# Kernel optimization log

Hardware: AMD Instinct MI355X
Metric: run time of the kernel (lower is better)

## Reference

```python
import jax, jax.numpy as jnp
import numpy as np

N_HEADS = 12

def setup_inputs() -> dict:
    key = jax.random.key(0)
    k1, k2, k3 = jax.random.split(key, 3)
    B, N, D = 2, 2048, 768
    x = jax.random.normal(k1, (B, N, D), dtype=jnp.float32)
    # Linear weights stored as [in, out] (equivalent to torch W.T)
    Wkqv = jax.random.normal(k2, (D, 3 * D), dtype=jnp.float32) * (1.0 / np.sqrt(D))
    bkqv = jnp.zeros((3 * D,), dtype=jnp.float32)
    Wproj = jax.random.normal(k3, (D, D), dtype=jnp.float32) * (1.0 / np.sqrt(D))
    bproj = jnp.zeros((D,), dtype=jnp.float32)
    return {"x": x, "Wkqv": Wkqv, "bkqv": bkqv, "Wproj": Wproj, "bproj": bproj}


def reference(x, Wkqv, bkqv, Wproj, bproj):
    B, N, D = x.shape
    H = N_HEADS
    hd = D // H
    kqv = x @ Wkqv + bkqv                     # [B, N, 3D]
    # NOTE: original chunks in (k, q, v) order
    k, q, v = jnp.split(kqv, 3, axis=-1)
    k = k.reshape(B, N, H, hd).transpose(0, 2, 1, 3)   # [B, H, N, hd]
    q = q.reshape(B, N, H, hd).transpose(0, 2, 1, 3)
    v = v.reshape(B, N, H, hd).transpose(0, 2, 1, 3)
    att = jnp.einsum('bhqd,bhkd->bhqk', q, k) / jnp.sqrt(jnp.float32(hd))
    causal = jnp.tril(jnp.ones((N, N), dtype=bool))    # [N, N]
    att = jnp.where(causal[None, None, :, :], att, jnp.float32(-jnp.inf))
    w = jax.nn.softmax(att, axis=-1)
    sa = jnp.einsum('bhqk,bhkd->bhqd', w, v)           # [B, H, N, hd]
    sa = sa.transpose(0, 2, 1, 3).reshape(B, N, D)
    return sa @ Wproj + bproj
```

## Files before the change

### kernel.cpp

```cpp
#include <hip/hip_runtime.h>

typedef __attribute__((ext_vector_type(8))) short bf16x8;
typedef __attribute__((ext_vector_type(4))) float f32x4;
typedef __attribute__((ext_vector_type(16))) float f32x16;

#define BATCH 2
#define SEQ 2048
#define DMODEL 768
#define NH 12
#define HD 64
#define M_TOK (BATCH * SEQ)
#define N_KQV (3 * DMODEL)

#define GLOAD16(gsrc, ldst) __builtin_amdgcn_global_load_lds( \
    (const __attribute__((address_space(1))) unsigned int*)(const void*)(gsrc), \
    (__attribute__((address_space(3))) unsigned int*)(void*)(ldst), 16, 0, 0)

__device__ __forceinline__ unsigned short f2bf(float f) {
  unsigned int u = __float_as_uint(f);
  u += 0x7FFFu + ((u >> 16) & 1u);
  return (unsigned short)(u >> 16);
}

__device__ __forceinline__ unsigned int cvtpk(float lo, float hi) {
  unsigned int r;
  asm("v_cvt_pk_bf16_f32 %0, %1, %2" : "=v"(r) : "v"(lo), "v"(hi));
  return r;
}


__global__ void cvt_f32_bf16(const float* __restrict__ in,
                             unsigned short* __restrict__ out, int n4) {
  int i = blockIdx.x * blockDim.x + threadIdx.x;
  if (i >= n4) return;
  float4 v = reinterpret_cast<const float4*>(in)[i];
  unsigned long long p = (unsigned long long)f2bf(v.x)
                       | ((unsigned long long)f2bf(v.y) << 16)
                       | ((unsigned long long)f2bf(v.z) << 32)
                       | ((unsigned long long)f2bf(v.w) << 48);
  reinterpret_cast<unsigned long long*>(out)[i] = p;
}

__global__ void transpose_cvt(const float* __restrict__ in,
                              unsigned short* __restrict__ out,
                              int rows, int cols) {
  __shared__ float tile[32][33];
  int c0 = blockIdx.x * 32, r0 = blockIdx.y * 32;
  for (int i = threadIdx.y; i < 32; i += 8)
    tile[i][threadIdx.x] = in[(size_t)(r0 + i) * cols + c0 + threadIdx.x];
  __syncthreads();
  for (int i = threadIdx.y; i < 32; i += 8)
    out[(size_t)(c0 + i) * rows + r0 + threadIdx.x] = f2bf(tile[threadIdx.x][i]);
}

template <int MODE>
__global__ __launch_bounds__(256) void gemm_bt(
    const unsigned short* __restrict__ A,
    const unsigned short* __restrict__ BT,
    const float* __restrict__ bias,
    int M, int N, int K,
    unsigned short* __restrict__ outK, unsigned short* __restrict__ outQ,
    unsigned short* __restrict__ outVT, float* __restrict__ outF) {
  __shared__ __align__(16) unsigned short lds_a[2][128][32];
  __shared__ __align__(16) unsigned short lds_b[2][128][32];
  const int tid = threadIdx.x;
  const int lane = tid & 63;
  const int w = tid >> 6;
  const int wm = w >> 1, wn = w & 1;
  const int l15 = lane & 15, lg = lane >> 4;
  const int m0 = blockIdx.y * 128, n0 = blockIdx.x * 128;

  f32x4 acc[4][4];
#pragma unroll
  for (int i = 0; i < 4; i++)
#pragma unroll
    for (int jj = 0; jj < 4; jj++) acc[i][jj] = (f32x4){0.f, 0.f, 0.f, 0.f};

  const int grow = lane >> 2;
  const int gcol = (lane & 3) * 8;

  const int KT = K >> 5;

#define STAGE_TILE(buf, k0)                                                  \
  {                                                                          \
    const size_t a0 = (size_t)(m0 + w * 32 + grow) * K + (k0) + gcol;        \
    const size_t b0 = (size_t)(n0 + w * 32 + grow) * K + (k0) + gcol;        \
    GLOAD16(&A[a0],                  &lds_a[buf][w * 32][0]);                \
    GLOAD16(&A[a0 + 16 * (size_t)K], &lds_a[buf][w * 32 + 16][0]);           \
    GLOAD16(&BT[b0],                 &lds_b[buf][w * 32][0]);                \
    GLOAD16(&BT[b0 + 16 * (size_t)K], &lds_b[buf][w * 32 + 16][0]);          \
  }

  STAGE_TILE(0, 0);
  __syncthreads();

  for (int kt = 0; kt < KT; ++kt) {
    const int cur = kt & 1;
    if (kt + 1 < KT) STAGE_TILE(cur ^ 1, (kt + 1) << 5);
    bf16x8 af[4], bfr[4];
#pragma unroll
    for (int mi = 0; mi < 4; mi++)
      af[mi] = *(const bf16x8*)&lds_a[cur][wm * 64 + mi * 16 + l15][lg * 8];
#pragma unroll
    for (int ni = 0; ni < 4; ni++)
      bfr[ni] = *(const bf16x8*)&lds_b[cur][wn * 64 + ni * 16 + l15][lg * 8];
#pragma unroll
    for (int mi = 0; mi < 4; mi++)
#pragma unroll
      for (int ni = 0; ni < 4; ni++)
        acc[mi][ni] = __builtin_amdgcn_mfma_f32_16x16x32_bf16(af[mi], bfr[ni], acc[mi][ni], 0, 0, 0);
    __syncthreads();
  }
#undef STAGE_TILE

#pragma unroll
  for (int mi = 0; mi < 4; mi++) {
#pragma unroll
    for (int ni = 0; ni < 4; ni++) {
#pragma unroll
      for (int r = 0; r < 4; r++) {
        int row = m0 + wm * 64 + mi * 16 + lg * 4 + r;
        int col = n0 + wn * 64 + ni * 16 + l15;
        float v = acc[mi][ni][r] + bias[col];
        if (MODE == 0) {
          int chunk = col / DMODEL;
          int d = col - chunk * DMODEL;
          int hh = d >> 6, di = d & 63;
          int bb = row >> 11, tok = row & 2047;
          int bh = bb * NH + hh;
          if (chunk == 0)
            outK[((size_t)bh * SEQ + tok) * HD + di] = f2bf(v);
          else if (chunk == 1)
            outQ[((size_t)bh * SEQ + tok) * HD + di] = f2bf(v * 0.125f);
          else
            outVT[((size_t)bh * HD + di) * SEQ + tok] = f2bf(v);
        } else {
          outF[(size_t)row * N + col] = v;
        }
      }
    }
  }
}

__global__ __launch_bounds__(128) void attn_kernel(
    const unsigned short* __restrict__ qbuf,
    const unsigned short* __restrict__ kbuf,
    const unsigned short* __restrict__ vT,
    unsigned short* __restrict__ sa) {
  __shared__ __align__(16) char smem_raw[18432];
  auto k_lds = reinterpret_cast<unsigned short (*)[72]>(smem_raw);
  auto v_lds = reinterpret_cast<unsigned short (*)[72]>(smem_raw + 9216);
  auto o_merge = reinterpret_cast<float (*)[32][33]>(smem_raw);
  auto l_merge = reinterpret_cast<float (*)[32]>(smem_raw + 9216);

  const int tid = threadIdx.x, lane = tid & 63, w = tid >> 6;
  const int l31 = lane & 31, hi = lane >> 5;

  const int fid = (int)blockIdx.y * (int)gridDim.x + (int)blockIdx.x;
  const int xcd = fid & 7, slot = fid >> 3;
  const int bh = ((slot >> 6) << 3) + xcd;
  const int t = 63 - (slot & 63);
  const int ktmax = t >> 1;

  const size_t qk_base = (size_t)bh * SEQ * HD;
  const size_t v_base = (size_t)bh * HD * SEQ;
  const int bb = bh / NH, h = bh - bb * NH;

  const int sr = w * 32 + (lane >> 3);
  const int sc = (lane & 7) * 8;

  {
    bf16x8 rk[4], rv[4];
#pragma unroll
    for (int p = 0; p < 4; p++) {
      rk[p] = *(const bf16x8*)&kbuf[qk_base + (size_t)(sr + 8 * p) * HD + sc];
      rv[p] = *(const bf16x8*)&vT[v_base + (size_t)(sr + 8 * p) * SEQ + sc];
    }
#pragma unroll
    for (int p = 0; p < 4; p++) {
      *(bf16x8*)&k_lds[sr + 8 * p][sc] = rk[p];
      *(bf16x8*)&v_lds[sr + 8 * p][sc] = rv[p];
    }
  }

  bf16x8 aq[4];
#pragma unroll
  for (int ds = 0; ds < 4; ds++)
    aq[ds] = *(const bf16x8*)&qbuf[qk_base + (size_t)(t * 32 + l31) * HD + ds * 16 + hi * 8];

  f32x16 o0, o1;
#pragma unroll
  for (int i = 0; i < 16; i++) { o0[i] = 0.f; o1[i] = 0.f; }
  float lsum = 0.f;

  __syncthreads();

  for (int kt = 0; kt <= ktmax; ++kt) {
    const bool more = (kt < ktmax);
    bf16x8 rk[4], rv[4];
    if (more) {
      const int nrow = (kt + 1) * 64;
#pragma unroll
      for (int p = 0; p < 4; p++) {
        rk[p] = *(const bf16x8*)&kbuf[qk_base + (size_t)(nrow + sr + 8 * p) * HD + sc];
        rv[p] = *(const bf16x8*)&vT[v_base + (size_t)(sr + 8 * p) * SEQ + nrow + sc];
      }
    }

    f32x16 s;
#pragma unroll
    for (int i = 0; i < 16; i++) s[i] = 0.f;
    __builtin_amdgcn_s_setprio(1);
#pragma unroll
    for (int ds = 0; ds < 4; ds++) {
      bf16x8 bk = *(const bf16x8*)&k_lds[w * 32 + l31][ds * 16 + hi * 8];
      s = __builtin_amdgcn_mfma_f32_32x32x16_bf16(bk, aq[ds], s, 0, 0, 0);
    }
    __builtin_amdgcn_s_setprio(0);

    const bool diag = (kt == ktmax);
    const int qb2 = (t & 1) * 32;
#pragma unroll
    for (int r = 0; r < 16; r++) {
      int kr = (r & 3) + 8 * (r >> 2) + 4 * hi;
      float val = s[r];
      if (diag && (w * 32 + kr > qb2 + l31)) val = -1e30f;
      float p = __expf(val);
      s[r] = p;
      lsum += p;
    }

    union { unsigned int u[4]; bf16x8 v; } f1, f2;
    {
      unsigned int A = cvtpk(s[0], s[1]), B = cvtpk(s[2], s[3]);
      unsigned int C = cvtpk(s[4], s[5]), D = cvtpk(s[6], s[7]);
      auto rAC = __builtin_amdgcn_permlane32_swap(A, C, false, false);
      auto rBD = __builtin_amdgcn_permlane32_swap(B, D, false, false);
      f1.u[0] = rAC[0]; f1.u[1] = rBD[0]; f1.u[2] = rAC[1]; f1.u[3] = rBD[1];
      unsigned int A2 = cvtpk(s[8], s[9]),   B2 = cvtpk(s[10], s[11]);
      unsigned int C2 = cvtpk(s[12], s[13]), D2 = cvtpk(s[14], s[15]);
      auto rAC2 = __builtin_amdgcn_permlane32_swap(A2, C2, false, false);
      auto rBD2 = __builtin_amdgcn_permlane32_swap(B2, D2, false, false);
      f2.u[0] = rAC2[0]; f2.u[1] = rBD2[0]; f2.u[2] = rAC2[1]; f2.u[3] = rBD2[1];
    }

    __builtin_amdgcn_s_setprio(1);
    {
      bf16x8 bv00 = *(const bf16x8*)&v_lds[l31][w * 32 + hi * 8];
      bf16x8 bv01 = *(const bf16x8*)&v_lds[32 + l31][w * 32 + hi * 8];
      o0 = __builtin_amdgcn_mfma_f32_32x32x16_bf16(f1.v, bv00, o0, 0, 0, 0);
      o1 = __builtin_amdgcn_mfma_f32_32x32x16_bf16(f1.v, bv01, o1, 0, 0, 0);
      bf16x8 bv10 = *(const bf16x8*)&v_lds[l31][w * 32 + 16 + hi * 8];
      bf16x8 bv11 = *(const bf16x8*)&v_lds[32 + l31][w * 32 + 16 + hi * 8];
      o0 = __builtin_amdgcn_mfma_f32_32x32x16_bf16(f2.v, bv10, o0, 0, 0, 0);
      o1 = __builtin_amdgcn_mfma_f32_32x32x16_bf16(f2.v, bv11, o1, 0, 0, 0);
    }
    __builtin_amdgcn_s_setprio(0);

    if (more) {
      __syncthreads();
#pragma unroll
      for (int p = 0; p < 4; p++) {
        *(bf16x8*)&k_lds[sr + 8 * p][sc] = rk[p];
        *(bf16x8*)&v_lds[sr + 8 * p][sc] = rv[p];
      }
      __syncthreads();
    }
  }

  __syncthreads();
  {
    float ltot = lsum + __shfl_xor(lsum, 32);
    if (hi == 0) l_merge[w][l31] = ltot;
    f32x16 osend = w ? o0 : o1;
#pragma unroll
    for (int r = 0; r < 16; r++) {
      int ql = (r & 3) + 8 * (r >> 2) + 4 * hi;
      o_merge[w][ql][l31] = osend[r];
    }
    __syncthreads();
    f32x16 okeep = w ? o1 : o0;
#pragma unroll
    for (int r = 0; r < 16; r++) {
      int ql = (r & 3) + 8 * (r >> 2) + 4 * hi;
      float ot = okeep[r] + o_merge[1 - w][ql][l31];
      float lt = l_merge[0][ql] + l_merge[1][ql];
      sa[((size_t)bb * SEQ + t * 32 + ql) * DMODEL + h * HD + w * 32 + l31] = f2bf(ot / lt);
    }
  }
}


extern "C" void kernel_launch(void* const* d_in, const int* in_sizes, int n_in,
                              void* d_out, int out_size, void* d_ws, size_t ws_size,
                              hipStream_t stream) {
  const float* x     = (const float*)d_in[0];
  const float* Wkqv  = (const float*)d_in[1];
  const float* bkqv  = (const float*)d_in[2];
  const float* Wproj = (const float*)d_in[3];
  const float* bproj = (const float*)d_in[4];
  float* out = (float*)d_out;

  char* ws = (char*)d_ws;
  unsigned short* x_bf   = (unsigned short*)(ws + 0);
  unsigned short* wkqvT  = (unsigned short*)(ws + 6291456);
  unsigned short* wprojT = (unsigned short*)(ws + 9830400);
  unsigned short* qb     = (unsigned short*)(ws + 11010048);
  unsigned short* kb     = (unsigned short*)(ws + 17301504);
  unsigned short* vT     = (unsigned short*)(ws + 23592960);
  unsigned short* sa     = (unsigned short*)(ws + 29884416);

  cvt_f32_bf16<<<(M_TOK * DMODEL / 4 + 255) / 256, 256, 0, stream>>>(x, x_bf, M_TOK * DMODEL / 4);
  transpose_cvt<<<dim3(N_KQV / 32, DMODEL / 32), dim3(32, 8), 0, stream>>>(Wkqv, wkqvT, DMODEL, N_KQV);
  transpose_cvt<<<dim3(DMODEL / 32, DMODEL / 32), dim3(32, 8), 0, stream>>>(Wproj, wprojT, DMODEL, DMODEL);

  gemm_bt<0><<<dim3(N_KQV / 128, M_TOK / 128), 256, 0, stream>>>(
      x_bf, wkqvT, bkqv, M_TOK, N_KQV, DMODEL, kb, qb, vT, nullptr);

  attn_kernel<<<dim3(64, BATCH * NH), 128, 0, stream>>>(qb, kb, vT, sa);

  gemm_bt<1><<<dim3(DMODEL / 128, M_TOK / 128), 256, 0, stream>>>(
      sa, wprojT, bproj, M_TOK, DMODEL, DMODEL, nullptr, nullptr, nullptr, out);
}
```

Measured before the change: 113.2 us.

## Give each wave its own 32 query rows and double-buffer K/V tiles in LDS

Restructures the attention kernel so each block handles 64 query rows, with each of two waves owning 32 rows and iterating over both 32-key halves of every 64-key tile. This replaces the old key-split across waves and removes the end-of-kernel cross-wave merge of O and row sums. K/V tiles are now double-buffered in LDS, cutting one barrier per iteration, and fully masked diagonal sub-tiles are skipped. The grid halves to 768 blocks, which lowers parallelism and uses more LDS per block.

```diff
diff --git a/kernel.cpp b/kernel.cpp
--- a/kernel.cpp
+++ b/kernel.cpp
@@ -147,20 +147,19 @@
     const unsigned short* __restrict__ kbuf,
     const unsigned short* __restrict__ vT,
     unsigned short* __restrict__ sa) {
-  __shared__ __align__(16) char smem_raw[18432];
-  auto k_lds = reinterpret_cast<unsigned short (*)[72]>(smem_raw);
-  auto v_lds = reinterpret_cast<unsigned short (*)[72]>(smem_raw + 9216);
-  auto o_merge = reinterpret_cast<float (*)[32][33]>(smem_raw);
-  auto l_merge = reinterpret_cast<float (*)[32]>(smem_raw + 9216);
+  __shared__ __align__(16) unsigned short k_lds[2][64][72];
+  __shared__ __align__(16) unsigned short v_lds[2][64][72];
+  __shared__ float l_sh[2][32];
 
   const int tid = threadIdx.x, lane = tid & 63, w = tid >> 6;
   const int l31 = lane & 31, hi = lane >> 5;
 
   const int fid = (int)blockIdx.y * (int)gridDim.x + (int)blockIdx.x;
   const int xcd = fid & 7, slot = fid >> 3;
-  const int bh = ((slot >> 6) << 3) + xcd;
-  const int t = 63 - (slot & 63);
-  const int ktmax = t >> 1;
+  const int head3 = slot % 3;
+  const int t = 31 - slot / 3;
+  const int bh = head3 * 8 + xcd;
+  const int ktmax = t;
 
   const size_t qk_base = (size_t)bh * SEQ * HD;
   const size_t v_base = (size_t)bh * HD * SEQ;
@@ -178,25 +177,28 @@
     }
 #pragma unroll
     for (int p = 0; p < 4; p++) {
-      *(bf16x8*)&k_lds[sr + 8 * p][sc] = rk[p];
-      *(bf16x8*)&v_lds[sr + 8 * p][sc] = rv[p];
+      *(bf16x8*)&k_lds[0][sr + 8 * p][sc] = rk[p];
+      *(bf16x8*)&v_lds[0][sr + 8 * p][sc] = rv[p];
     }
   }
 
   bf16x8 aq[4];
 #pragma unroll
   for (int ds = 0; ds < 4; ds++)
-    aq[ds] = *(const bf16x8*)&qbuf[qk_base + (size_t)(t * 32 + l31) * HD + ds * 16 + hi * 8];
+    aq[ds] = *(const bf16x8*)&qbuf[qk_base + (size_t)(t * 64 + w * 32 + l31) * HD + ds * 16 + hi * 8];
 
   f32x16 o0, o1;
 #pragma unroll
   for (int i = 0; i < 16; i++) { o0[i] = 0.f; o1[i] = 0.f; }
-  float lsum = 0.f;
+  float ls0 = 0.f, ls1 = 0.f;
 
   __syncthreads();
 
   for (int kt = 0; kt <= ktmax; ++kt) {
+    const int cur = kt & 1;
     const bool more = (kt < ktmax);
+    const bool diag = (kt == ktmax);
+
     bf16x8 rk[4], rv[4];
     if (more) {
       const int nrow = (kt + 1) * 64;
@@ -207,85 +209,81 @@
       }
     }
 
-    f32x16 s;
-#pragma unroll
-    for (int i = 0; i < 16; i++) s[i] = 0.f;
-    __builtin_amdgcn_s_setprio(1);
-#pragma unroll
-    for (int ds = 0; ds < 4; ds++) {
-      bf16x8 bk = *(const bf16x8*)&k_lds[w * 32 + l31][ds * 16 + hi * 8];
-      s = __builtin_amdgcn_mfma_f32_32x32x16_bf16(bk, aq[ds], s, 0, 0, 0);
-    }
-    __builtin_amdgcn_s_setprio(0);
-
-    const bool diag = (kt == ktmax);
-    const int qb2 = (t & 1) * 32;
-#pragma unroll
-    for (int r = 0; r < 16; r++) {
-      int kr = (r & 3) + 8 * (r >> 2) + 4 * hi;
-      float val = s[r];
-      if (diag && (w * 32 + kr > qb2 + l31)) val = -1e30f;
-      float p = __expf(val);
-      s[r] = p;
-      lsum += p;
-    }
-
-    union { unsigned int u[4]; bf16x8 v; } f1, f2;
-    {
-      unsigned int A = cvtpk(s[0], s[1]), B = cvtpk(s[2], s[3]);
-      unsigned int C = cvtpk(s[4], s[5]), D = cvtpk(s[6], s[7]);
-      auto rAC = __builtin_amdgcn_permlane32_swap(A, C, false, false);
-      auto rBD = __builtin_amdgcn_permlane32_swap(B, D, false, false);
-      f1.u[0] = rAC[0]; f1.u[1] = rBD[0]; f1.u[2] = rAC[1]; f1.u[3] = rBD[1];
-      unsigned int A2 = cvtpk(s[8], s[9]),   B2 = cvtpk(s[10], s[11]);
-      unsigned int C2 = cvtpk(s[12], s[13]), D2 = cvtpk(s[14], s[15]);
-      auto rAC2 = __builtin_amdgcn_permlane32_swap(A2, C2, false, false);
-      auto rBD2 = __builtin_amdgcn_permlane32_swap(B2, D2, false, false);
-      f2.u[0] = rAC2[0]; f2.u[1] = rBD2[0]; f2.u[2] = rAC2[1]; f2.u[3] = rBD2[1];
-    }
-
-    __builtin_amdgcn_s_setprio(1);
-    {
-      bf16x8 bv00 = *(const bf16x8*)&v_lds[l31][w * 32 + hi * 8];
-      bf16x8 bv01 = *(const bf16x8*)&v_lds[32 + l31][w * 32 + hi * 8];
-      o0 = __builtin_amdgcn_mfma_f32_32x32x16_bf16(f1.v, bv00, o0, 0, 0, 0);
-      o1 = __builtin_amdgcn_mfma_f32_32x32x16_bf16(f1.v, bv01, o1, 0, 0, 0);
-      bf16x8 bv10 = *(const bf16x8*)&v_lds[l31][w * 32 + 16 + hi * 8];
-      bf16x8 bv11 = *(const bf16x8*)&v_lds[32 + l31][w * 32 + 16 + hi * 8];
-      o0 = __builtin_amdgcn_mfma_f32_32x32x16_bf16(f2.v, bv10, o0, 0, 0, 0);
-      o1 = __builtin_amdgcn_mfma_f32_32x32x16_bf16(f2.v, bv11, o1, 0, 0, 0);
-    }
-    __builtin_amdgcn_s_setprio(0);
+#pragma unroll
+    for (int kh = 0; kh < 2; kh++) {
+      if (diag && kh > w) continue;
+
+      f32x16 s;
+#pragma unroll
+      for (int i = 0; i < 16; i++) s[i] = 0.f;
+      __builtin_amdgcn_s_setprio(1);
+#pragma unroll
+      for (int ds = 0; ds < 4; ds++) {
+        bf16x8 bk = *(const bf16x8*)&k_lds[cur][kh * 32 + l31][ds * 16 + hi * 8];
+        s = __builtin_amdgcn_mfma_f32_32x32x16_bf16(bk, aq[ds], s, 0, 0, 0);
+      }
+      __builtin_amdgcn_s_setprio(0);
+
+      const bool dmask = diag && (kh == w);
+#pragma unroll
+      for (int r = 0; r < 16; r++) {
+        int kr = (r & 3) + 8 * (r >> 2) + 4 * hi;
+        float val = s[r];
+        if (dmask && kr > l31) val = -1e30f;
+        float p = __expf(val);
+        s[r] = p;
+        if (r & 1) ls1 += p; else ls0 += p;
+      }
+
+      union { unsigned int u[4]; bf16x8 v; } f1, f2;
+      {
+        unsigned int A = cvtpk(s[0], s[1]), B = cvtpk(s[2], s[3]);
+        unsigned int C = cvtpk(s[4], s[5]), D = cvtpk(s[6], s[7]);
+        auto rAC = __builtin_amdgcn_permlane32_swap(A, C, false, false);
+        auto rBD = __builtin_amdgcn_permlane32_swap(B, D, false, false);
+        f1.u[0] = rAC[0]; f1.u[1] = rBD[0]; f1.u[2] = rAC[1]; f1.u[3] = rBD[1];
+        unsigned int A2 = cvtpk(s[8], s[9]),   B2 = cvtpk(s[10], s[11]);
+        unsigned int C2 = cvtpk(s[12], s[13]), D2 = cvtpk(s[14], s[15]);
+        auto rAC2 = __builtin_amdgcn_permlane32_swap(A2, C2, false, false);
+        auto rBD2 = __builtin_amdgcn_permlane32_swap(B2, D2, false, false);
+        f2.u[0] = rAC2[0]; f2.u[1] = rBD2[0]; f2.u[2] = rAC2[1]; f2.u[3] = rBD2[1];
+      }
+
+      __builtin_amdgcn_s_setprio(1);
+      {
+        bf16x8 bv00 = *(const bf16x8*)&v_lds[cur][l31][kh * 32 + hi * 8];
+        bf16x8 bv01 = *(const bf16x8*)&v_lds[cur][32 + l31][kh * 32 + hi * 8];
+        o0 = __builtin_amdgcn_mfma_f32_32x32x16_bf16(f1.v, bv00, o0, 0, 0, 0);
+        o1 = __builtin_amdgcn_mfma_f32_32x32x16_bf16(f1.v, bv01, o1, 0, 0, 0);
+        bf16x8 bv10 = *(const bf16x8*)&v_lds[cur][l31][kh * 32 + 16 + hi * 8];
+        bf16x8 bv11 = *(const bf16x8*)&v_lds[cur][32 + l31][kh * 32 + 16 + hi * 8];
+        o0 = __builtin_amdgcn_mfma_f32_32x32x16_bf16(f2.v, bv10, o0, 0, 0, 0);
+        o1 = __builtin_amdgcn_mfma_f32_32x32x16_bf16(f2.v, bv11, o1, 0, 0, 0);
+      }
+      __builtin_amdgcn_s_setprio(0);
+    }
 
     if (more) {
+#pragma unroll
+      for (int p = 0; p < 4; p++) {
+        *(bf16x8*)&k_lds[cur ^ 1][sr + 8 * p][sc] = rk[p];
+        *(bf16x8*)&v_lds[cur ^ 1][sr + 8 * p][sc] = rv[p];
+      }
       __syncthreads();
-#pragma unroll
-      for (int p = 0; p < 4; p++) {
-        *(bf16x8*)&k_lds[sr + 8 * p][sc] = rk[p];
-        *(bf16x8*)&v_lds[sr + 8 * p][sc] = rv[p];
-      }
-      __syncthreads();
-    }
-  }
-
-  __syncthreads();
+    }
+  }
+
   {
-    float ltot = lsum + __shfl_xor(lsum, 32);
-    if (hi == 0) l_merge[w][l31] = ltot;
-    f32x16 osend = w ? o0 : o1;
+    float lt = ls0 + ls1;
+    lt += __shfl_xor(lt, 32);
+    if (hi == 0) l_sh[w][l31] = lt;
 #pragma unroll
     for (int r = 0; r < 16; r++) {
       int ql = (r & 3) + 8 * (r >> 2) + 4 * hi;
-      o_merge[w][ql][l31] = osend[r];
-    }
-    __syncthreads();
-    f32x16 okeep = w ? o1 : o0;
-#pragma unroll
-    for (int r = 0; r < 16; r++) {
-      int ql = (r & 3) + 8 * (r >> 2) + 4 * hi;
-      float ot = okeep[r] + o_merge[1 - w][ql][l31];
-      float lt = l_merge[0][ql] + l_merge[1][ql];
-      sa[((size_t)bb * SEQ + t * 32 + ql) * DMODEL + h * HD + w * 32 + l31] = f2bf(ot / lt);
+      float inv = 1.0f / l_sh[w][ql];
+      size_t row = (size_t)bb * SEQ + t * 64 + w * 32 + ql;
+      sa[row * DMODEL + h * HD + l31]      = f2bf(o0[r] * inv);
+      sa[row * DMODEL + h * HD + 32 + l31] = f2bf(o1[r] * inv);
     }
   }
 }
@@ -317,7 +315,7 @@
   gemm_bt<0><<<dim3(N_KQV / 128, M_TOK / 128), 256, 0, stream>>>(
       x_bf, wkqvT, bkqv, M_TOK, N_KQV, DMODEL, kb, qb, vT, nullptr);
 
-  attn_kernel<<<dim3(64, BATCH * NH), 128, 0, stream>>>(qb, kb, vT, sa);
+  attn_kernel<<<dim3(32, BATCH * NH), 128, 0, stream>>>(qb, kb, vT, sa);
 
   gemm_bt<1><<<dim3(DMODEL / 128, M_TOK / 128), 256, 0, stream>>>(
       sa, wprojT, bproj, M_TOK, DMODEL, DMODEL, nullptr, nullptr, nullptr, out);
```

After: 124.8 us. 10.2% more time.
